# Optimization experiments

Hardware: AMD Instinct MI355X
Metric: run time of the kernel (lower is better)

The kernel has to match this reference:

```python
import jax, jax.numpy as jnp
import numpy as np

N_NEURONS = 512
N_HID = 3
N_CLASSES = 2
BATCH = 512
NS = 150


def setup_inputs() -> dict:
    key = jax.random.key(0)
    ks = jax.random.split(key, 15)
    s = 1.0 / np.sqrt(N_NEURONS)
    s2 = 1.0 / np.sqrt(N_CLASSES)
    return {
        "x": jax.random.normal(ks[0], (BATCH, N_NEURONS), jnp.float32),
        # stacked hidden-layer params (3 layers of 512x512)
        "mu_Wh": jax.random.normal(ks[1], (N_HID, N_NEURONS, N_NEURONS), jnp.float32) * s,
        "v_Wh": jax.random.normal(ks[2], (N_HID, N_NEURONS, N_NEURONS), jnp.float32) * 0.05 - 2.0,
        "vo_Wh": jax.random.normal(ks[3], (N_HID, N_NEURONS, N_NEURONS), jnp.float32) * s,
        "vi_Wh": jax.random.normal(ks[4], (N_HID, N_NEURONS, N_NEURONS), jnp.float32) * s,
        "mu_bh": jax.random.normal(ks[5], (N_HID, N_NEURONS), jnp.float32) * 0.1,
        "v_bh": jax.random.normal(ks[6], (N_HID, N_NEURONS), jnp.float32) * 0.05 - 2.0,
        "vb_bh": jax.random.normal(ks[7], (N_HID, N_NEURONS, N_NEURONS), jnp.float32) * s,
        "mu_Wo": jax.random.normal(ks[8], (N_CLASSES, N_NEURONS), jnp.float32) * s,
        "v_Wo": jax.random.normal(ks[9], (N_CLASSES, N_NEURONS), jnp.float32) * 0.05 - 2.0,
        "vo_Wo": jax.random.normal(ks[10], (N_CLASSES, N_CLASSES), jnp.float32) * s2,
        "vi_Wo": jax.random.normal(ks[11], (N_NEURONS, N_NEURONS), jnp.float32) * s,
        "mu_bo": jax.random.normal(ks[12], (N_CLASSES,), jnp.float32) * 0.1,
        "v_bo": jax.random.normal(ks[13], (N_CLASSES,), jnp.float32) * 0.05 - 2.0,
        "vb_bo": jax.random.normal(ks[14], (N_CLASSES, N_CLASSES), jnp.float32) * s2,
        "ns": NS,
    }


def reference(x, mu_Wh, v_Wh, vo_Wh, vi_Wh, mu_bh, v_bh, vb_bh,
              mu_Wo, v_Wo, vo_Wo, vi_Wo, mu_bo, v_bo, vb_bo, ns):
    def sample_forward(key):
        k = jax.random.split(key, 4)
        # r = randn_like(m) * sqrt(exp(2v)); rp = vo @ r @ vi.T (KFAC projection)
        rWh = jax.random.normal(k[0], v_Wh.shape, v_Wh.dtype) * jnp.sqrt(jnp.exp(2.0 * v_Wh))
        tmp = jnp.einsum('loa,lab->lob', vo_Wh, rWh)
        Wh = jnp.einsum('lob,lib->loi', tmp, vi_Wh) + mu_Wh          # [3, 512, 512]
        rbh = jax.random.normal(k[1], v_bh.shape, v_bh.dtype) * jnp.sqrt(jnp.exp(2.0 * v_bh))
        bh = jnp.einsum('loa,la->lo', vb_bh, rbh) + mu_bh            # [3, 512]
        rWo = jax.random.normal(k[2], v_Wo.shape, v_Wo.dtype) * jnp.sqrt(jnp.exp(2.0 * v_Wo))
        Wo = vo_Wo @ rWo @ vi_Wo.T + mu_Wo                           # [2, 512]
        rbo = jax.random.normal(k[3], v_bo.shape, v_bo.dtype) * jnp.sqrt(jnp.exp(2.0 * v_bo))
        bo = vb_bo @ rbo + mu_bo                                     # [2]
        h = x
        for l in range(N_HID):  # fixed small layer count
            h = jax.nn.relu(h @ Wh[l].T + bh[l])
        return h @ Wo.T + bo                                         # [B, 2]

    keys = jax.random.split(jax.random.key(42), ns)
    _, ys = jax.lax.scan(lambda c, k: (c, sample_forward(k)), None, keys)
    return ys  # [ns, B, 2]
```

## Files before the change

kernel.cpp:

```cpp
#include <hip/hip_runtime.h>
#include <hip/hip_bf16.h>
#include <stdint.h>


#define NSAMP 150

typedef unsigned int u32;
typedef unsigned short ushort_t;
using short8 = __attribute__((ext_vector_type(8))) short;
using us8    = __attribute__((ext_vector_type(8))) unsigned short;
using us4    = __attribute__((ext_vector_type(4))) unsigned short;
using f32x4  = __attribute__((ext_vector_type(4))) float;

__device__ __forceinline__ u32 rotl32(u32 x, int r){ return (x<<r)|(x>>(32-r)); }

__device__ __forceinline__ void tf_block(u32 k0, u32 k1, u32 x0, u32 x1, u32& o0, u32& o1){
  u32 k2 = k0 ^ k1 ^ 0x1BD11BDAu;
  x0 += k0; x1 += k1;
#define TF_R4(a,b,c,d) \
  x0+=x1; x1=rotl32(x1,a); x1^=x0; \
  x0+=x1; x1=rotl32(x1,b); x1^=x0; \
  x0+=x1; x1=rotl32(x1,c); x1^=x0; \
  x0+=x1; x1=rotl32(x1,d); x1^=x0;
  TF_R4(13,15,26,6)  x0+=k1; x1+=k2+1u;
  TF_R4(17,29,16,24) x0+=k2; x1+=k0+2u;
  TF_R4(13,15,26,6)  x0+=k0; x1+=k1+3u;
  TF_R4(17,29,16,24) x0+=k1; x1+=k2+4u;
  TF_R4(13,15,26,6)  x0+=k2; x1+=k0+5u;
#undef TF_R4
  o0=x0; o1=x1;
}

__device__ __forceinline__ u32 jax_bits(u32 kh, u32 kl, u32 e){
  u32 o0,o1; tf_block(kh,kl,0u,e,o0,o1); return o0^o1;
}

__device__ __forceinline__ float erfinv_xla(float x){
  float w = -log1pf(-x*x);
  float p;
  if (w < 5.0f) {
    w -= 2.5f;
    p =              2.81022636e-08f;
    p = fmaf(p, w,   3.43273939e-07f);
    p = fmaf(p, w,  -3.5233877e-06f);
    p = fmaf(p, w,  -4.39150654e-06f);
    p = fmaf(p, w,   0.00021858087f);
    p = fmaf(p, w,  -0.00125372503f);
    p = fmaf(p, w,  -0.00417768164f);
    p = fmaf(p, w,   0.246640727f);
    p = fmaf(p, w,   1.50140941f);
  } else {
    w = sqrtf(w) - 3.0f;
    p =             -0.000200214257f;
    p = fmaf(p, w,   0.000100950558f);
    p = fmaf(p, w,   0.00134934322f);
    p = fmaf(p, w,  -0.00367342844f);
    p = fmaf(p, w,   0.00573950773f);
    p = fmaf(p, w,  -0.0076224613f);
    p = fmaf(p, w,   0.00943887047f);
    p = fmaf(p, w,   1.00167406f);
    p = fmaf(p, w,   2.83297682f);
  }
  return p * x;
}

__device__ __forceinline__ float erfinv_fast(float x){
  float y = (1.0f - x) * (1.0f + x);
  float w = -0.6931471805599453f * __log2f(y);
  float p;
  if (w < 5.0f) {
    float t = w - 2.5f;
    p =              2.81022636e-08f;
    p = fmaf(p, t,   3.43273939e-07f);
    p = fmaf(p, t,  -3.5233877e-06f);
    p = fmaf(p, t,  -4.39150654e-06f);
    p = fmaf(p, t,   0.00021858087f);
    p = fmaf(p, t,  -0.00125372503f);
    p = fmaf(p, t,  -0.00417768164f);
    p = fmaf(p, t,   0.246640727f);
    p = fmaf(p, t,   1.50140941f);
  } else {
    float t = __fsqrt_rn(w) - 3.0f;
    p =             -0.000200214257f;
    p = fmaf(p, t,   0.000100950558f);
    p = fmaf(p, t,   0.00134934322f);
    p = fmaf(p, t,  -0.00367342844f);
    p = fmaf(p, t,   0.00573950773f);
    p = fmaf(p, t,  -0.0076224613f);
    p = fmaf(p, t,   0.00943887047f);
    p = fmaf(p, t,   1.00167406f);
    p = fmaf(p, t,   2.83297682f);
  }
  return p * x;
}

__device__ __forceinline__ float bits_to_uniform(u32 bits){
  float f = __uint_as_float((bits >> 9) | 0x3F800000u) - 1.0f;
  const float lo = -0.99999994f;
  float u = fmaf(f, 2.0f, lo);
  return fmaxf(u, lo);
}

__device__ __forceinline__ float bits_to_normal(u32 bits){
  return 1.41421356237f * erfinv_xla(bits_to_uniform(bits));
}
__device__ __forceinline__ float bits_to_normal_fast(u32 bits){
  return 1.41421356237f * erfinv_fast(bits_to_uniform(bits));
}

__device__ __forceinline__ ushort_t f2bf(float x){
  u32 u = __float_as_uint(x);
  u32 r = (u + 0x7FFFu + ((u>>16)&1u)) >> 16;
  return (ushort_t)r;
}
__device__ __forceinline__ float bf2f(ushort_t u){ return __uint_as_float(((u32)u)<<16); }

__device__ __forceinline__ void gload16(const void* g, void* l){
  __builtin_amdgcn_global_load_lds((const __attribute__((address_space(1))) void*)g,
                                   (__attribute__((address_space(3))) void*)l, 16, 0, 0);
}

__global__ void k_keys(u32* __restrict__ keys){
  int s = threadIdx.x;
  if (s >= NSAMP) return;
  u32 sh, sl;
  tf_block(0u,42u,0u,(u32)s,sh,sl);
  u32* k = keys + s*8;
  tf_block(sh,sl,0u,0u,k[0],k[1]);
  tf_block(sh,sl,0u,1u,k[2],k[3]);
  tf_block(sh,sl,0u,2u,k[4],k[5]);
  tf_block(sh,sl,0u,3u,k[6],k[7]);
}

__global__ void k_sigt(const float* __restrict__ v, float* __restrict__ sT){
  __shared__ float tile[32][33];
  int lw = blockIdx.z;
  int a0 = blockIdx.y*32, b0 = blockIdx.x*32;
  const float* src = v + (size_t)lw*262144;
  #pragma unroll
  for (int i=0;i<4;++i){
    int a = a0 + threadIdx.y + i*8;
    tile[threadIdx.y + i*8][threadIdx.x] = src[(size_t)a*512 + b0 + threadIdx.x];
  }
  __syncthreads();
  float* dst = sT + (size_t)lw*262144;
  #pragma unroll
  for (int i=0;i<4;++i){
    int b = b0 + threadIdx.y + i*8;
    float vv = tile[threadIdx.x][threadIdx.y + i*8];
    dst[(size_t)b*512 + a0 + threadIdx.x] = sqrtf(expf(2.f*vv));
  }
}

__global__ __launch_bounds__(256) void k_cvt(const float* __restrict__ in,
                                             ushort_t* __restrict__ out){
  int i = (blockIdx.x*256 + threadIdx.x)*4;
  float4 v = *(const float4*)(in + i);
  us4 o; o[0]=f2bf(v.x); o[1]=f2bf(v.y); o[2]=f2bf(v.z); o[3]=f2bf(v.w);
  *(us4*)(out + i) = o;
}

__global__ __launch_bounds__(256) void k_genrw(const float* __restrict__ sigT,
                                               const u32* __restrict__ keys,
                                               ushort_t* __restrict__ rWT, int s0){
  int sl = blockIdx.x / 384;
  int bi = blockIdx.x - sl*384;
  int q  = bi*256 + threadIdx.x;
  int f0 = q*8;
  int lw = f0 >> 18;
  int r  = f0 & 262143;
  int b  = r >> 9;
  int a0 = r & 511;
  const u32* k = keys + (size_t)(s0+sl)*8;
  u32 kh=k[0], kl=k[1];
  u32 eb = (u32)(lw*262144 + a0*512 + b);
  float4 sa = *(const float4*)(sigT + f0);
  float4 sb = *(const float4*)(sigT + f0 + 4);
  float ss[8] = {sa.x,sa.y,sa.z,sa.w,sb.x,sb.y,sb.z,sb.w};
  us8 o;
  #pragma unroll
  for (int j=0;j<8;++j){
    float n = bits_to_normal_fast(jax_bits(kh,kl, eb + (u32)(j*512)));
    o[j] = f2bf(n * ss[j]);
  }
  *(us8*)(rWT + (size_t)sl*786432 + f0) = o;
}

__global__ __launch_bounds__(512) void k_small(const float* __restrict__ mu_bh,
                                               const float* __restrict__ v_bh,
                                               const float* __restrict__ vb_bh,
                                               const float* __restrict__ mu_Wo,
                                               const float* __restrict__ v_Wo,
                                               const float* __restrict__ vo_Wo,
                                               const float* __restrict__ vi_Wo,
                                               const float* __restrict__ mu_bo,
                                               const float* __restrict__ v_bo,
                                               const float* __restrict__ vb_bo,
                                               const u32* __restrict__ keys,
                                               float* __restrict__ bh_all,
                                               float* __restrict__ Wo_all,
                                               float* __restrict__ bo_all){
  int s = blockIdx.x, t = threadIdx.x;
  const u32* k = keys + (size_t)s*8;
  __shared__ __align__(16) float rbh[1536];
  __shared__ __align__(16) float t2[1024];
  for (int e=t; e<1536; e+=512)
    rbh[e] = bits_to_normal(jax_bits(k[2],k[3],(u32)e)) * sqrtf(expf(2.f*v_bh[e]));
  {
    float r0 = bits_to_normal(jax_bits(k[4],k[5],(u32)t))       * sqrtf(expf(2.f*v_Wo[t]));
    float r1 = bits_to_normal(jax_bits(k[4],k[5],(u32)(t+512))) * sqrtf(expf(2.f*v_Wo[t+512]));
    t2[t]     = vo_Wo[0]*r0 + vo_Wo[1]*r1;
    t2[t+512] = vo_Wo[2]*r0 + vo_Wo[3]*r1;
  }
  __syncthreads();
  for (int e=t; e<1536; e+=512){
    int lw = e >> 9;
    const float* row = vb_bh + (size_t)e*512;
    const float* rb = rbh + (lw<<9);
    float acc = 0.f;
    for (int a=0;a<512;a+=4){
      float4 vv = *(const float4*)(row+a);
      acc += vv.x*rb[a] + vv.y*rb[a+1] + vv.z*rb[a+2] + vv.w*rb[a+3];
    }
    bh_all[(size_t)s*1536+e] = acc + mu_bh[e];
  }
  {
    const float* row = vi_Wo + (size_t)t*512;
    float a0=0.f, a1=0.f;
    for (int b=0;b<512;b+=4){
      float4 vv = *(const float4*)(row+b);
      a0 += vv.x*t2[b]    +vv.y*t2[b+1]    +vv.z*t2[b+2]    +vv.w*t2[b+3];
      a1 += vv.x*t2[512+b]+vv.y*t2[512+b+1]+vv.z*t2[512+b+2]+vv.w*t2[512+b+3];
    }
    Wo_all[(size_t)s*1024 + t]       = a0 + mu_Wo[t];
    Wo_all[(size_t)s*1024 + 512 + t] = a1 + mu_Wo[512+t];
  }
  if (t < 2){
    float rb0 = bits_to_normal(jax_bits(k[6],k[7],0u)) * sqrtf(expf(2.f*v_bo[0]));
    float rb1 = bits_to_normal(jax_bits(k[6],k[7],1u)) * sqrtf(expf(2.f*v_bo[1]));
    bo_all[(size_t)s*2+t] = vb_bo[t*2+0]*rb0 + vb_bo[t*2+1]*rb1 + mu_bo[t];
  }
}

template<int EPI>
__device__ __forceinline__ void gemm_core(const ushort_t* __restrict__ A,
                                          const ushort_t* __restrict__ B,
                                          const float* __restrict__ E,
                                          ushort_t* __restrict__ C){
  __shared__ ushort_t As[4096];
  __shared__ ushort_t Bs[4096];
  const int t = threadIdx.x;
  const int l = t & 63;
  const int m0 = blockIdx.y * 128, n0 = blockIdx.x * 128;
  const int wr = (t >> 7) & 1, wc = (t >> 6) & 1;
  const int srow = t >> 2, scol = (t & 3) << 3;
  const ushort_t* Ag = A + (size_t)(m0 + srow) * 512 + scol;
  const ushort_t* Bg = B + (size_t)(n0 + srow) * 512 + scol;
  ushort_t* Al = As + t * 8;
  ushort_t* Bl = Bs + t * 8;
  const int rfr = l & 15, kfr = (l >> 4) << 3;
  f32x4 acc[4][4] = {};
  for (int k0 = 0; k0 < 512; k0 += 32) {
    gload16(Ag + k0, Al);
    gload16(Ag + 64*512 + k0, Al + 2048);
    gload16(Bg + k0, Bl);
    gload16(Bg + 64*512 + k0, Bl + 2048);
    __syncthreads();
    short8 af[4], bfv[4];
    #pragma unroll
    for (int i=0;i<4;++i){
      af[i]  = *(const short8*)(As + (wr*64 + i*16 + rfr)*32 + kfr);
      bfv[i] = *(const short8*)(Bs + (wc*64 + i*16 + rfr)*32 + kfr);
    }
    #pragma unroll
    for (int i=0;i<4;++i)
      #pragma unroll
      for (int j=0;j<4;++j)
        acc[i][j] = __builtin_amdgcn_mfma_f32_16x16x32_bf16(af[i], bfv[j], acc[i][j], 0, 0, 0);
    __syncthreads();
  }
  const int cr = (l >> 4) << 2, cc = l & 15;
  #pragma unroll
  for (int i=0;i<4;++i){
    #pragma unroll
    for (int j=0;j<4;++j){
      int row = m0 + wr*64 + i*16 + cr;
      int col = n0 + wc*64 + j*16 + cc;
      #pragma unroll
      for (int r=0;r<4;++r){
        float v = acc[i][j][r];
        if (EPI==1) v += E[(size_t)(row+r)*512 + col];
        if (EPI==2) v = fmaxf(v + E[col], 0.f);
        C[(size_t)(row+r)*512 + col] = f2bf(v);
      }
    }
  }
}

__global__ __launch_bounds__(256) void k_tmp(const ushort_t* __restrict__ vo,
                                             const ushort_t* __restrict__ rWT,
                                             ushort_t* __restrict__ tmp){
  int z = blockIdx.z, lw = z % 3;
  gemm_core<0>(vo + (size_t)lw*262144, rWT + (size_t)z*262144, nullptr,
               tmp + (size_t)z*262144);
}

__global__ __launch_bounds__(256) void k_wh(const ushort_t* __restrict__ tmp,
                                            const ushort_t* __restrict__ vi,
                                            const float* __restrict__ mu,
                                            ushort_t* __restrict__ Wh){
  int z = blockIdx.z, lw = z % 3;
  gemm_core<1>(tmp + (size_t)z*262144, vi + (size_t)lw*262144,
               mu + (size_t)lw*262144, Wh + (size_t)z*262144);
}

__global__ __launch_bounds__(256) void k_fwd(const ushort_t* __restrict__ xbf,
                                             const ushort_t* __restrict__ Wh,
                                             const float* __restrict__ bh_all,
                                             ushort_t* __restrict__ hb, int lw, int s0){
  int sl = blockIdx.z;
  ushort_t* hbase = hb + (size_t)sl*786432;
  const ushort_t* A = (lw==0) ? xbf : (hbase + (lw==2 ? 262144 : 0));
  ushort_t* O = hbase + (lw==1 ? 262144 : 0);
  gemm_core<2>(A, Wh + (size_t)(sl*3+lw)*262144,
               bh_all + (size_t)(s0+sl)*1536 + (size_t)lw*512, O);
}

__global__ __launch_bounds__(256) void k_out(const ushort_t* __restrict__ hb,
                                             const float* __restrict__ Wo_all,
                                             const float* __restrict__ bo_all,
                                             float* __restrict__ out, int s0){
  int sl = blockIdx.x;
  int b = blockIdx.y*256 + threadIdx.x;
  const ushort_t* h = hb + (size_t)sl*786432 + (size_t)b*512;
  int s = s0 + sl;
  const float* W0 = Wo_all + (size_t)s*1024;
  const float* W1 = W0 + 512;
  float a0=0.f, a1=0.f;
  for (int i=0;i<512;i+=8){
    us8 hv = *(const us8*)(h+i);
    #pragma unroll
    for (int j=0;j<8;++j){
      float hf = bf2f(hv[j]);
      a0 = fmaf(hf, W0[i+j], a0);
      a1 = fmaf(hf, W1[i+j], a1);
    }
  }
  out[((size_t)s*512 + b)*2 + 0] = a0 + bo_all[(size_t)s*2+0];
  out[((size_t)s*512 + b)*2 + 1] = a1 + bo_all[(size_t)s*2+1];
}

extern "C" void kernel_launch(void* const* d_in, const int* in_sizes, int n_in,
                              void* d_out, int out_size, void* d_ws, size_t ws_size,
                              hipStream_t stream){
  const float* x      = (const float*)d_in[0];
  const float* mu_Wh  = (const float*)d_in[1];
  const float* v_Wh   = (const float*)d_in[2];
  const float* vo_Wh  = (const float*)d_in[3];
  const float* vi_Wh  = (const float*)d_in[4];
  const float* mu_bh  = (const float*)d_in[5];
  const float* v_bh   = (const float*)d_in[6];
  const float* vb_bh  = (const float*)d_in[7];
  const float* mu_Wo  = (const float*)d_in[8];
  const float* v_Wo   = (const float*)d_in[9];
  const float* vo_Wo  = (const float*)d_in[10];
  const float* vi_Wo  = (const float*)d_in[11];
  const float* mu_bo  = (const float*)d_in[12];
  const float* v_bo   = (const float*)d_in[13];
  const float* vb_bo  = (const float*)d_in[14];
  float* out = (float*)d_out;

  char* ws = (char*)d_ws;
  u32*      keys   = (u32*)(ws + 0);
  float*    bh_all = (float*)(ws + 8192);
  float*    Wo_all = (float*)(ws + 929792);
  float*    bo_all = (float*)(ws + 1544192);
  float*    sigT   = (float*)(ws + 1546240);
  ushort_t* vo_bf  = (ushort_t*)(ws + 4691968);
  ushort_t* vi_bf  = (ushort_t*)(ws + 6264832);
  ushort_t* xbf    = (ushort_t*)(ws + 7837696);
  const size_t big_off = 8388608;
  const size_t per_sample_b = 2u * 1572864u;
  size_t avail = (ws_size > big_off) ? (ws_size - big_off) : 0;
  int C = (int)(avail / per_sample_b);
  if (C < 1) C = 1;
  if (C > NSAMP) C = NSAMP;
  ushort_t* bufRW = (ushort_t*)(ws + big_off);
  ushort_t* bufT  = bufRW + (size_t)C*786432;

  hipLaunchKernelGGL(k_keys, dim3(1), dim3(256), 0, stream, keys);
  hipLaunchKernelGGL(k_small, dim3(NSAMP), dim3(512), 0, stream,
                     mu_bh, v_bh, vb_bh, mu_Wo, v_Wo, vo_Wo, vi_Wo,
                     mu_bo, v_bo, vb_bo, keys, bh_all, Wo_all, bo_all);
  hipLaunchKernelGGL(k_sigt, dim3(16,16,3), dim3(32,8), 0, stream, v_Wh, sigT);
  hipLaunchKernelGGL(k_cvt, dim3(768), dim3(256), 0, stream, vo_Wh, vo_bf);
  hipLaunchKernelGGL(k_cvt, dim3(768), dim3(256), 0, stream, vi_Wh, vi_bf);
  hipLaunchKernelGGL(k_cvt, dim3(256), dim3(256), 0, stream, x, xbf);

  for (int s0 = 0; s0 < NSAMP; s0 += C){
    int Cc = (NSAMP - s0 < C) ? (NSAMP - s0) : C;
    hipLaunchKernelGGL(k_genrw, dim3(Cc*384), dim3(256), 0, stream, sigT, keys, bufRW, s0);
    hipLaunchKernelGGL(k_tmp, dim3(4,4,Cc*3), dim3(256), 0, stream, vo_bf, bufRW, bufT);
    hipLaunchKernelGGL(k_wh,  dim3(4,4,Cc*3), dim3(256), 0, stream, bufT, vi_bf, mu_Wh, bufRW);
    for (int lw = 0; lw < 3; ++lw)
      hipLaunchKernelGGL(k_fwd, dim3(4,4,Cc), dim3(256), 0, stream, xbf, bufRW, bh_all, bufT, lw, s0);
    hipLaunchKernelGGL(k_out, dim3(Cc,2), dim3(256), 0, stream, bufT, Wo_all, bo_all, out, s0);
  }
  (void)in_sizes; (void)n_in; (void)out_size;
}
```

Before: 1.202 ms.

## Fuse the two KFAC projection GEMMs into one kernel with an LDS intermediate

Replaces the separate vo@r and tmp@vi^T GEMM kernels with a single kernel. Each block computes a 128-row strip of tmp in 128-column chunks, stages each chunk as bf16 in shared memory, and immediately multiplies it by vi to accumulate the full 128x512 Wh strip, adding mu in the epilogue. This removes the global write and re-read of the tmp intermediate and one launch per chunk. In exchange, each block holds a large accumulator (32 f32x4 per thread), which raises register pressure. The vi operand is read straight from global memory without LDS staging, and the grid has fewer, larger blocks, which may lower occupancy.

```diff
diff --git a/kernel.cpp b/kernel.cpp
--- a/kernel.cpp
+++ b/kernel.cpp
@@ -242,6 +242,80 @@
   }
 }
 
+__global__ __launch_bounds__(512) void k_whf(const ushort_t* __restrict__ vo,
+                                             const ushort_t* __restrict__ vi,
+                                             const float* __restrict__ mu,
+                                             const ushort_t* __restrict__ rWT,
+                                             ushort_t* __restrict__ Wh){
+  __shared__ ushort_t A1s[4096];
+  __shared__ ushort_t B1s[4096];
+  __shared__ ushort_t Ts[128*136];
+  const int z = blockIdx.y, lw = z % 3;
+  const ushort_t* VO = vo  + (size_t)lw*262144;
+  const ushort_t* VI = vi  + (size_t)lw*262144;
+  const float*    MU = mu  + (size_t)lw*262144;
+  const ushort_t* RW = rWT + (size_t)z*262144;
+  ushort_t*      WHO = Wh  + (size_t)z*262144;
+  const int m0 = blockIdx.x * 128;
+  const int t = threadIdx.x, l = t & 63, w = t >> 6;
+  const int wm = w >> 2, wi = w & 3;
+  const int srow = t >> 2, scol = (t & 3) << 3;
+  const int rfr = l & 15, kfr = (l >> 4) << 3;
+  const int cr = (l >> 4) << 2, cc = l & 15;
+  f32x4 acc2[4][8] = {};
+  for (int nb = 0; nb < 4; ++nb){
+    const int b0 = nb * 128;
+    f32x4 acc1[4][2] = {};
+    for (int k0 = 0; k0 < 512; k0 += 32){
+      gload16(VO + (size_t)(m0 + srow)*512 + k0 + scol, A1s + t*8);
+      gload16(RW + (size_t)(b0 + srow)*512 + k0 + scol, B1s + t*8);
+      __syncthreads();
+      short8 af[4], bf[2];
+      #pragma unroll
+      for (int i=0;i<4;++i) af[i] = *(const short8*)(A1s + (wm*64 + i*16 + rfr)*32 + kfr);
+      #pragma unroll
+      for (int j=0;j<2;++j) bf[j] = *(const short8*)(B1s + (wi*32 + j*16 + rfr)*32 + kfr);
+      #pragma unroll
+      for (int i=0;i<4;++i)
+        #pragma unroll
+        for (int j=0;j<2;++j)
+          acc1[i][j] = __builtin_amdgcn_mfma_f32_16x16x32_bf16(af[i], bf[j], acc1[i][j], 0,0,0);
+      __syncthreads();
+    }
+    #pragma unroll
+    for (int i=0;i<4;++i)
+      #pragma unroll
+      for (int j=0;j<2;++j)
+        #pragma unroll
+        for (int r=0;r<4;++r)
+          Ts[(wm*64 + i*16 + cr + r)*136 + wi*32 + j*16 + cc] = f2bf(acc1[i][j][r]);
+    __syncthreads();
+    for (int kk = 0; kk < 128; kk += 32){
+      short8 a2[4];
+      #pragma unroll
+      for (int i=0;i<4;++i) a2[i] = *(const short8*)(Ts + (wm*64 + i*16 + rfr)*136 + kk + kfr);
+      #pragma unroll
+      for (int j=0;j<8;++j){
+        short8 b2 = *(const short8*)(VI + (size_t)(wi*128 + j*16 + rfr)*512 + b0 + kk + kfr);
+        #pragma unroll
+        for (int i=0;i<4;++i)
+          acc2[i][j] = __builtin_amdgcn_mfma_f32_16x16x32_bf16(a2[i], b2, acc2[i][j], 0,0,0);
+      }
+    }
+    __syncthreads();
+  }
+  #pragma unroll
+  for (int i=0;i<4;++i)
+    #pragma unroll
+    for (int j=0;j<8;++j)
+      #pragma unroll
+      for (int r=0;r<4;++r){
+        int row = m0 + wm*64 + i*16 + cr + r;
+        int col = wi*128 + j*16 + cc;
+        WHO[(size_t)row*512 + col] = f2bf(acc2[i][j][r] + MU[(size_t)row*512 + col]);
+      }
+}
+
 template<int EPI>
 __device__ __forceinline__ void gemm_core(const ushort_t* __restrict__ A,
                                           const ushort_t* __restrict__ B,
@@ -289,29 +363,11 @@
       #pragma unroll
       for (int r=0;r<4;++r){
         float v = acc[i][j][r];
-        if (EPI==1) v += E[(size_t)(row+r)*512 + col];
         if (EPI==2) v = fmaxf(v + E[col], 0.f);
         C[(size_t)(row+r)*512 + col] = f2bf(v);
       }
     }
   }
-}
-
-__global__ __launch_bounds__(256) void k_tmp(const ushort_t* __restrict__ vo,
-                                             const ushort_t* __restrict__ rWT,
-                                             ushort_t* __restrict__ tmp){
-  int z = blockIdx.z, lw = z % 3;
-  gemm_core<0>(vo + (size_t)lw*262144, rWT + (size_t)z*262144, nullptr,
-               tmp + (size_t)z*262144);
-}
-
-__global__ __launch_bounds__(256) void k_wh(const ushort_t* __restrict__ tmp,
-                                            const ushort_t* __restrict__ vi,
-                                            const float* __restrict__ mu,
-                                            ushort_t* __restrict__ Wh){
-  int z = blockIdx.z, lw = z % 3;
-  gemm_core<1>(tmp + (size_t)z*262144, vi + (size_t)lw*262144,
-               mu + (size_t)lw*262144, Wh + (size_t)z*262144);
 }
 
 __global__ __launch_bounds__(256) void k_fwd(const ushort_t* __restrict__ xbf,
@@ -400,11 +456,11 @@
   for (int s0 = 0; s0 < NSAMP; s0 += C){
     int Cc = (NSAMP - s0 < C) ? (NSAMP - s0) : C;
     hipLaunchKernelGGL(k_genrw, dim3(Cc*384), dim3(256), 0, stream, sigT, keys, bufRW, s0);
-    hipLaunchKernelGGL(k_tmp, dim3(4,4,Cc*3), dim3(256), 0, stream, vo_bf, bufRW, bufT);
-    hipLaunchKernelGGL(k_wh,  dim3(4,4,Cc*3), dim3(256), 0, stream, bufT, vi_bf, mu_Wh, bufRW);
+    hipLaunchKernelGGL(k_whf, dim3(4, Cc*3), dim3(512), 0, stream,
+                       vo_bf, vi_bf, mu_Wh, bufRW, bufT);
     for (int lw = 0; lw < 3; ++lw)
-      hipLaunchKernelGGL(k_fwd, dim3(4,4,Cc), dim3(256), 0, stream, xbf, bufRW, bh_all, bufT, lw, s0);
-    hipLaunchKernelGGL(k_out, dim3(Cc,2), dim3(256), 0, stream, bufT, Wo_all, bo_all, out, s0);
+      hipLaunchKernelGGL(k_fwd, dim3(4,4,Cc), dim3(256), 0, stream, xbf, bufT, bh_all, bufRW, lw, s0);
+    hipLaunchKernelGGL(k_out, dim3(Cc,2), dim3(256), 0, stream, bufRW, Wo_all, bo_all, out, s0);
   }
   (void)in_sizes; (void)n_in; (void)out_size;
 }
```

New measurement: 1.630 ms. +35.6%, slower.
